# Kernel optimization log

Hardware: AMD Instinct MI355X
Metric: run time of the kernel (lower is better)

Reference implementation:

```python
import jax, jax.numpy as jnp
import numpy as np

B, C, H, W = 8, 256, 128, 128
KC, VC, HEADS = 256, 256, 2
HK, HV = KC // HEADS, VC // HEADS
EPS = 1e-5


def setup_inputs() -> dict:
    key = jax.random.key(0)
    ks = jax.random.split(key, 10)
    s = 0.02  # init scale for weights
    return {
        "x": jax.random.normal(ks[0], (B, C, H, W), jnp.float32),
        "bn_gamma": jnp.ones((C,), jnp.float32),
        "bn_beta": jnp.zeros((C,), jnp.float32),
        "wk": jax.random.normal(ks[1], (KC, C), jnp.float32) * s,
        "bk": jnp.zeros((KC,), jnp.float32),
        "wq": jax.random.normal(ks[2], (KC, C), jnp.float32) * s,
        "bq": jnp.zeros((KC,), jnp.float32),
        "wv": jax.random.normal(ks[3], (VC, C), jnp.float32) * s,
        "bv": jnp.zeros((VC,), jnp.float32),
        "w_fc1": jax.random.normal(ks[4], (HEADS, HEADS), jnp.float32) * 0.5,
        "b_fc1": jnp.zeros((HEADS,), jnp.float32),
        "w_fc2": jax.random.normal(ks[5], (HEADS, HEADS), jnp.float32) * 0.5,
        "b_fc2": jnp.zeros((HEADS,), jnp.float32),
        "w_se": jax.random.normal(ks[6], (HEADS,), jnp.float32) * 0.5,  # Conv2d(heads,1,1) weight
        "b_se": jnp.zeros((), jnp.float32),
        "w_rep": jax.random.normal(ks[7], (C, C), jnp.float32) * s,
        "b_rep": jnp.zeros((C,), jnp.float32),
    }


def reference(x, bn_gamma, bn_beta, wk, bk, wq, bq, wv, bv,
              w_fc1, b_fc1, w_fc2, b_fc2, w_se, b_se, w_rep, b_rep):
    n, c, h, w = x.shape
    s = h * w
    # BatchNorm2d (training-mode math: batch statistics over N,H,W)
    mean = x.mean(axis=(0, 2, 3))
    var = x.var(axis=(0, 2, 3))
    xn = (x - mean[None, :, None, None]) * jax.lax.rsqrt(var + EPS)[None, :, None, None]
    xn = xn * bn_gamma[None, :, None, None] + bn_beta[None, :, None, None]
    xr = xn.reshape(n, c, s)  # [B, C, HW]
    # 1x1 convs == per-pixel channel matmuls
    k = jnp.einsum('oc,bcs->bos', wk, xr) + bk[None, :, None]
    q = jnp.einsum('oc,bcs->bos', wq, xr) + bq[None, :, None]
    v = jnp.einsum('oc,bcs->bos', wv, xr) + bv[None, :, None]
    # split heads: [B, HEADS, hk, S]
    k = jax.nn.softmax(k.reshape(n, HEADS, HK, s), axis=-1)   # softmax over spatial
    q = jax.nn.softmax(q.reshape(n, HEADS, HK, s), axis=2)    # softmax over channel
    v = v.reshape(n, HEADS, HV, s)
    # linear-attention context: key @ value^T -> [B, HEADS, hk, hv]
    context = jnp.einsum('bnks,bnvs->bnkv', k, v)
    # SE block over head channel (in_channels = HEADS, reduction = 1)
    pooled = context.mean(axis=(2, 3))                              # [B, HEADS]
    gate = jax.nn.sigmoid(jax.nn.relu(pooled @ w_fc1.T + b_fc1) @ w_fc2.T + b_fc2)
    gated = context * gate[:, :, None, None]
    ctx = jnp.einsum('n,bnkv->bkv', w_se, gated) + b_se             # Conv2d(HEADS,1,1): [B, hk, hv]
    # second pass: ctx^T @ query per head, concat over heads -> [B, C, S]
    out = jnp.einsum('bkv,bnks->bnvs', ctx, q).reshape(n, c, s)
    out = jnp.einsum('oc,bcs->bos', w_rep, out) + b_rep[None, :, None]
    return out.reshape(n, c, h, w)
```

## Files before the change

### kernel.cpp

```cpp
#include <hip/hip_runtime.h>
#include <hip/hip_bf16.h>

#define BATCH 8
#define CH 256
#define SPAT 16384
#define TP 64
#define PITCH 272

typedef __attribute__((ext_vector_type(4))) float f32x4;
typedef __attribute__((ext_vector_type(8))) __bf16 bf16x8;
typedef __attribute__((ext_vector_type(4))) __bf16 bf16x4;

#define WS_ROWSUM  512
#define WS_POOLED  2560
#define WS_BKF     2576
#define WS_BQF     2832
#define WS_BVF     3088
#define WS_SUM     3344
#define WS_SSUM    3600
#define WS_CTX     4096
#define WS_MBF     266240
#define WS_WKBF    528384
#define WS_WQBF    561152
#define WS_WVBF    593920

__device__ __forceinline__ int lswz(int h) { return h ^ (((h >> 7) & 7) << 3); }

__device__ __forceinline__ void blockReduce2(float& a, float& b, volatile float* sm) {
    int lane = threadIdx.x & 63, w = threadIdx.x >> 6;
#pragma unroll
    for (int o = 32; o; o >>= 1) { a += __shfl_down(a, o); b += __shfl_down(b, o); }
    if (lane == 0) { sm[w] = a; sm[4 + w] = b; }
    __syncthreads();
    if (threadIdx.x == 0) {
        a = sm[0] + sm[1] + sm[2] + sm[3];
        b = sm[4] + sm[5] + sm[6] + sm[7];
    }
}

__global__ __launch_bounds__(256) void ea_bnstats(const float* __restrict__ x,
                                                  float* sums, float* ssums) {
    __shared__ float sm[8];
    int bi = blockIdx.x, c = bi >> 3, b = bi & 7;
    const float4* p = (const float4*)(x + (size_t)(b * CH + c) * SPAT);
    float sum = 0.f, ss = 0.f;
    for (int i = threadIdx.x; i < SPAT / 4; i += 256) {
        float4 v = p[i];
        sum += v.x + v.y + v.z + v.w;
        ss  += v.x * v.x + v.y * v.y + v.z * v.z + v.w * v.w;
    }
    blockReduce2(sum, ss, sm);
    if (threadIdx.x == 0) { atomicAdd(sums + c, sum); atomicAdd(ssums + c, ss); }
}

__global__ __launch_bounds__(256) void ea_fold(const float* __restrict__ wk, const float* __restrict__ wq,
        const float* __restrict__ wv, const float* __restrict__ bk, const float* __restrict__ bq,
        const float* __restrict__ bv, const float* __restrict__ gamma, const float* __restrict__ beta,
        const float* __restrict__ sums, const float* __restrict__ ssums,
        __bf16* wkb, __bf16* wqb, __bf16* wvb, float* bkf, float* bqf, float* bvf) {
    __shared__ float sm[12];
    int o = blockIdx.x, c = threadIdx.x;
    const float inv = 1.f / (float)(BATCH * SPAT);
    float mean = sums[c] * inv;
    float var  = ssums[c] * inv - mean * mean;
    float sc   = gamma[c] * rsqrtf(var + 1e-5f);
    float sh   = beta[c] - mean * sc;
    float k = wk[o * 256 + c], q = wq[o * 256 + c], v = wv[o * 256 + c];
    wkb[o * 256 + c] = (__bf16)(k * sc);
    wqb[o * 256 + c] = (__bf16)(q * sc);
    wvb[o * 256 + c] = (__bf16)(v * sc);
    float ak = k * sh, aq = q * sh, av = v * sh;
    int lane = c & 63, w = c >> 6;
#pragma unroll
    for (int off = 32; off; off >>= 1) {
        ak += __shfl_down(ak, off);
        aq += __shfl_down(aq, off);
        av += __shfl_down(av, off);
    }
    if (lane == 0) { sm[w] = ak; sm[4 + w] = aq; sm[8 + w] = av; }
    __syncthreads();
    if (c == 0) {
        bkf[o] = bk[o] + sm[0] + sm[1] + sm[2] + sm[3];
        bqf[o] = bq[o] + sm[4] + sm[5] + sm[6] + sm[7];
        bvf[o] = bv[o] + sm[8] + sm[9] + sm[10] + sm[11];
    }
}

__global__ __launch_bounds__(512, 2) void ea_kvctx(const float* __restrict__ x,
        const __bf16* __restrict__ wkb, const __bf16* __restrict__ wvb,
        const float* __restrict__ bkf, const float* __restrict__ bvf,
        float* __restrict__ ctx, float* __restrict__ rowsum) {
    __shared__ __bf16 Xl[2 * 64 * 256];
    __shared__ __bf16 Pl[256 * 64];
    __shared__ __bf16 Vl[256 * 64];
    const int bi = blockIdx.x, b = bi >> 5, chunk = bi & 31;
    const int t = threadIdx.x;
    const int lane = t & 63, wave = t >> 6, quad = lane >> 4, l15 = lane & 15;
    const int rbase = wave * 32;
    const int sl = t & 15, cg = t >> 4;
    const int xswz = (sl & 7) << 3;
    const float* xp0 = x + (size_t)(b * CH + cg * 8) * SPAT + chunk * 512 + 4 * sl;

    float bkr[2][4], bvr[2][4];
#pragma unroll
    for (int mt = 0; mt < 2; mt++)
#pragma unroll
        for (int r = 0; r < 4; r++) {
            int row = rbase + mt * 16 + quad * 4 + r;
            bkr[mt][r] = bkf[row];
            bvr[mt][r] = bvf[row];
        }

    const f32x4 z = {0.f, 0.f, 0.f, 0.f};
    f32x4 cacc[4][4];
#pragma unroll
    for (int mt = 0; mt < 4; mt++)
#pragma unroll
        for (int nt = 0; nt < 4; nt++) cacc[mt][nt] = z;
    float rs_acc[2][4] = {{0.f, 0.f, 0.f, 0.f}, {0.f, 0.f, 0.f, 0.f}};

    const int head = wave >> 2, rh = (wave >> 1) & 1, chh = wave & 1;
    const int prow0 = head * 128 + rh * 64, vrow0 = head * 128 + chh * 64;

    f32x4 xr[8];
#pragma unroll
    for (int i = 0; i < 8; i++) xr[i] = *(const f32x4*)(xp0 + (size_t)i * SPAT);
#pragma unroll
    for (int i = 0; i < 8; i++) {
        int ca = (cg * 8 + i) ^ xswz;
#pragma unroll
        for (int j = 0; j < 4; j++)
            Xl[(4 * sl + j) * 256 + ca] = (__bf16)xr[i][j];
    }
    __syncthreads();

    int buf = 0;
    for (int tt = 0; tt < 8; tt++) {
        if (tt < 7) {
            const float* xp = xp0 + (tt + 1) * 64;
#pragma unroll
            for (int i = 0; i < 8; i++) xr[i] = *(const f32x4*)(xp + (size_t)i * SPAT);
        }
        const __bf16* Xb = Xl + buf * (64 * 256);
        f32x4 ak[2][4], av[2][4];
#pragma unroll
        for (int mt = 0; mt < 2; mt++)
#pragma unroll
            for (int nt = 0; nt < 4; nt++) { ak[mt][nt] = z; av[mt][nt] = z; }
#pragma unroll 1
        for (int ks = 0; ks < 8; ks++) {
            int k0 = ks * 32 + quad * 8;
            bf16x8 bb[4];
#pragma unroll
            for (int nt = 0; nt < 4; nt++)
                bb[nt] = *(const bf16x8*)(Xb + (4 * l15 + nt) * 256 + (k0 ^ ((l15 & 7) << 3)));
            bf16x8 aK[2], aV[2];
#pragma unroll
            for (int mt = 0; mt < 2; mt++) {
                size_t off = (size_t)(rbase + mt * 16 + l15) * 256 + k0;
                aK[mt] = *(const bf16x8*)(wkb + off);
                aV[mt] = *(const bf16x8*)(wvb + off);
            }
#pragma unroll
            for (int mt = 0; mt < 2; mt++)
#pragma unroll
                for (int nt = 0; nt < 4; nt++) {
                    ak[mt][nt] = __builtin_amdgcn_mfma_f32_16x16x32_bf16(aK[mt], bb[nt], ak[mt][nt], 0, 0, 0);
                    av[mt][nt] = __builtin_amdgcn_mfma_f32_16x16x32_bf16(aV[mt], bb[nt], av[mt][nt], 0, 0, 0);
                }
        }
#pragma unroll
        for (int mt = 0; mt < 2; mt++)
#pragma unroll
            for (int r = 0; r < 4; r++) {
                int row = rbase + mt * 16 + quad * 4 + r;
                float bK = bkr[mt][r], bV = bvr[mt][r];
                float e0 = __expf(ak[mt][0][r] + bK);
                float e1 = __expf(ak[mt][1][r] + bK);
                float e2 = __expf(ak[mt][2][r] + bK);
                float e3 = __expf(ak[mt][3][r] + bK);
                rs_acc[mt][r] += e0 + e1 + e2 + e3;
                int pa = row * 64 + ((4 * l15) ^ ((row & 7) << 3));
                bf16x4 pk = {(__bf16)e0, (__bf16)e1, (__bf16)e2, (__bf16)e3};
                *(bf16x4*)(Pl + pa) = pk;
                bf16x4 vk = {(__bf16)(av[mt][0][r] + bV), (__bf16)(av[mt][1][r] + bV),
                             (__bf16)(av[mt][2][r] + bV), (__bf16)(av[mt][3][r] + bV)};
                *(bf16x4*)(Vl + pa) = vk;
            }
        __syncthreads();
        if (tt < 7) {
            __bf16* Xn = Xl + (buf ^ 1) * (64 * 256);
#pragma unroll
            for (int i = 0; i < 8; i++) {
                int ca = (cg * 8 + i) ^ xswz;
#pragma unroll
                for (int j = 0; j < 4; j++)
                    Xn[(4 * sl + j) * 256 + ca] = (__bf16)xr[i][j];
            }
        }
#pragma unroll
        for (int ks = 0; ks < 2; ks++) {
            int k0 = ks * 32 + quad * 8;
            bf16x8 pfr[4], vfr[4];
#pragma unroll
            for (int mt = 0; mt < 4; mt++) {
                int row = prow0 + mt * 16 + l15;
                pfr[mt] = *(const bf16x8*)(Pl + row * 64 + (k0 ^ ((row & 7) << 3)));
            }
#pragma unroll
            for (int nt = 0; nt < 4; nt++) {
                int row = vrow0 + nt * 16 + l15;
                vfr[nt] = *(const bf16x8*)(Vl + row * 64 + (k0 ^ ((row & 7) << 3)));
            }
#pragma unroll
            for (int mt = 0; mt < 4; mt++)
#pragma unroll
                for (int nt = 0; nt < 4; nt++)
                    cacc[mt][nt] = __builtin_amdgcn_mfma_f32_16x16x32_bf16(pfr[mt], vfr[nt], cacc[mt][nt], 0, 0, 0);
        }
        __syncthreads();
        buf ^= 1;
    }
#pragma unroll
    for (int mt = 0; mt < 2; mt++)
#pragma unroll
        for (int r = 0; r < 4; r++) {
            float v = rs_acc[mt][r];
            v += __shfl_xor(v, 1);
            v += __shfl_xor(v, 2);
            v += __shfl_xor(v, 4);
            v += __shfl_xor(v, 8);
            if (l15 == 0)
                atomicAdd(rowsum + b * CH + rbase + mt * 16 + quad * 4 + r, v);
        }
    float* cb = ctx + ((size_t)b * 2 + head) * 16384;
#pragma unroll
    for (int mt = 0; mt < 4; mt++)
#pragma unroll
        for (int nt = 0; nt < 4; nt++)
#pragma unroll
            for (int r = 0; r < 4; r++) {
                int kk = rh * 64 + mt * 16 + quad * 4 + r;
                int vv = chh * 64 + nt * 16 + l15;
                atomicAdd(cb + kk * 128 + vv, cacc[mt][nt][r]);
            }
}

__global__ void ea_normpool(float* ctx, const float* rowsum, float* pooled) {
    __shared__ float sm[8];
    int bi = blockIdx.x, b = bi >> 1, h = bi & 1;
    float* base = ctx + (size_t)bi * 16384;
    const float* rs = rowsum + b * CH + h * 128;
    float sum = 0.f, dummy = 0.f;
    for (int i = threadIdx.x; i < 16384; i += 256) {
        float v = base[i] / rs[i >> 7];
        base[i] = v;
        sum += v;
    }
    blockReduce2(sum, dummy, sm);
    if (threadIdx.x == 0) pooled[bi] = sum * (1.f / 16384.f);
}

__global__ __launch_bounds__(256) void ea_M(const float* ctx, const float* pooled,
                                            const float* wfc1, const float* bfc1,
                                            const float* wfc2, const float* bfc2,
                                            const float* wse, const float* bse,
                                            const float* wrep, __bf16* Mbf) {
    __shared__ float L[128 * 128];
    int bi = blockIdx.x, b = bi >> 3, h = (bi >> 2) & 1, strip = bi & 3;
    float p0 = pooled[b * 2], p1 = pooled[b * 2 + 1];
    float z10 = fmaxf(0.f, wfc1[0] * p0 + wfc1[1] * p1 + bfc1[0]);
    float z11 = fmaxf(0.f, wfc1[2] * p0 + wfc1[3] * p1 + bfc1[1]);
    float z20 = wfc2[0] * z10 + wfc2[1] * z11 + bfc2[0];
    float z21 = wfc2[2] * z10 + wfc2[3] * z11 + bfc2[1];
    float g0 = 1.f / (1.f + __expf(-z20)), g1 = 1.f / (1.f + __expf(-z21));
    float a0 = wse[0] * g0, a1 = wse[1] * g1, bs = bse[0];
    const float* c0 = ctx + (size_t)b * 2 * 16384;
    const float* c1 = c0 + 16384;
    for (int i = threadIdx.x; i < 16384; i += 256) L[i] = a0 * c0[i] + a1 * c1[i] + bs;
    __syncthreads();
    int o = strip * 64 + (threadIdx.x & 63), kb = (threadIdx.x >> 6) * 32;
    const float4* wr = (const float4*)(wrep + (size_t)o * 256 + h * 128);
    for (int kk = kb; kk < kb + 32; kk++) {
        const float4* Lr = (const float4*)(L + kk * 128);
        float acc = 0.f;
#pragma unroll 8
        for (int j = 0; j < 32; j++) {
            float4 w4 = wr[j];
            float4 l4 = Lr[j];
            acc += w4.x * l4.x + w4.y * l4.y + w4.z * l4.z + w4.w * l4.w;
        }
        Mbf[(size_t)(b * 256 + o) * 256 + h * 128 + kk] = (__bf16)acc;
    }
}

__device__ __forceinline__ void stage_x(const float* xb, __bf16* Xl, int t) {
    int l15 = t & 15, c0 = t >> 4;
    const float* xp = xb + l15 * 4;
    int hbase = (l15 * 4) * PITCH;
#pragma unroll
    for (int i = 0; i < 16; i++) {
        int c = c0 * 16 + i;
        float4 v = *(const float4*)(xp + (size_t)c * SPAT);
        Xl[lswz(hbase + c)]             = (__bf16)v.x;
        Xl[lswz(hbase + PITCH + c)]     = (__bf16)v.y;
        Xl[lswz(hbase + 2 * PITCH + c)] = (__bf16)v.z;
        Xl[lswz(hbase + 3 * PITCH + c)] = (__bf16)v.w;
    }
}

__device__ __forceinline__ void mm256(const __bf16* __restrict__ A, const __bf16* Xl,
                                      int WB, int quad, int l15, f32x4 (&acc)[4][4]) {
#pragma unroll 2
    for (int ks = 0; ks < 8; ks++) {
        int k0 = ks * 32;
        bf16x8 a[4];
#pragma unroll
        for (int mt = 0; mt < 4; mt++)
            a[mt] = *(const bf16x8*)(A + (WB + mt * 16 + l15) * 256 + k0 + quad * 8);
        bf16x8 bb[4];
#pragma unroll
        for (int nt = 0; nt < 4; nt++)
            bb[nt] = *(const bf16x8*)(Xl + lswz((4 * l15 + nt) * PITCH + k0 + quad * 8));
#pragma unroll
        for (int mt = 0; mt < 4; mt++)
#pragma unroll
            for (int nt = 0; nt < 4; nt++)
                acc[mt][nt] = __builtin_amdgcn_mfma_f32_16x16x32_bf16(a[mt], bb[nt], acc[mt][nt], 0, 0, 0);
    }
}

__global__ __launch_bounds__(256) void ea_final(const float* __restrict__ x,
        const __bf16* __restrict__ wqb, const float* __restrict__ bqf,
        const __bf16* __restrict__ Mbf, const float* __restrict__ brep, float* __restrict__ out) {
    __shared__ __bf16 X[TP * PITCH];
    __shared__ __bf16 Q[TP * PITCH];
    __shared__ float psum[256];
    __shared__ float rcp[TP * 2];
    int bi = blockIdx.x, b = bi >> 8, s0 = (bi & 255) * TP, t = threadIdx.x;
    stage_x(x + (size_t)b * CH * SPAT + s0, X, t);
    __syncthreads();

    int lane = t & 63, wave = t >> 6, quad = lane >> 4, l15 = lane & 15, WB = wave * 64;
    const f32x4 z = {0.f, 0.f, 0.f, 0.f};

    {
        f32x4 acc[4][4];
#pragma unroll
        for (int mt = 0; mt < 4; mt++)
#pragma unroll
            for (int nt = 0; nt < 4; nt++) acc[mt][nt] = z;
        mm256(wqb, X, WB, quad, l15, acc);
#pragma unroll
        for (int mt = 0; mt < 4; mt++) {
            int row0 = WB + mt * 16 + quad * 4;
#pragma unroll
            for (int nt = 0; nt < 4; nt++) {
                bf16x4 qk;
#pragma unroll
                for (int r = 0; r < 4; r++)
                    qk[r] = (__bf16)__expf(acc[mt][nt][r] + bqf[row0 + r]);
                *(bf16x4*)(Q + lswz((4 * l15 + nt) * PITCH + row0)) = qk;
            }
        }
    }
    __syncthreads();
    {
        int px = t & 63, hh = (t >> 6) & 1, part = t >> 7;
        int cb = hh * 128 + part * 64;
        float s = 0.f;
#pragma unroll
        for (int j = 0; j < 8; j++) {
            bf16x8 qv = *(const bf16x8*)(Q + lswz(px * PITCH + cb + j * 8));
#pragma unroll
            for (int e = 0; e < 8; e++) s += (float)qv[e];
        }
        psum[t] = s;
    }
    __syncthreads();
    if (t < 128) {
        float tot = psum[t] + psum[t + 128];
        rcp[(t & 63) * 2 + (t >> 6)] = 1.f / tot;
    }
    __syncthreads();
#pragma unroll 2
    for (int e = t; e < TP * 32; e += 256) {
        int px = e >> 5, cc = (e & 31) * 8;
        float sc = rcp[px * 2 + (cc >> 7)];
        int h = lswz(px * PITCH + cc);
        bf16x8 qv = *(const bf16x8*)(Q + h);
        bf16x8 qo;
#pragma unroll
        for (int j2 = 0; j2 < 8; j2++) qo[j2] = (__bf16)((float)qv[j2] * sc);
        *(bf16x8*)(Q + h) = qo;
    }
    __syncthreads();
    {
        f32x4 acc[4][4];
#pragma unroll
        for (int mt = 0; mt < 4; mt++)
#pragma unroll
            for (int nt = 0; nt < 4; nt++) acc[mt][nt] = z;
        mm256(Mbf + (size_t)b * 65536, Q, WB, quad, l15, acc);
#pragma unroll
        for (int mt = 0; mt < 4; mt++) {
            int row0 = WB + mt * 16 + quad * 4;
#pragma unroll
            for (int r = 0; r < 4; r++) {
                int row = row0 + r;
                float bs = brep[row];
                f32x4 o4 = {acc[mt][0][r] + bs, acc[mt][1][r] + bs,
                            acc[mt][2][r] + bs, acc[mt][3][r] + bs};
                *(f32x4*)(out + (size_t)(b * CH + row) * SPAT + s0 + 4 * l15) = o4;
            }
        }
    }
}

extern "C" void kernel_launch(void* const* d_in, const int* in_sizes, int n_in,
                              void* d_out, int out_size, void* d_ws, size_t ws_size,
                              hipStream_t stream) {
    (void)in_sizes; (void)n_in; (void)out_size; (void)ws_size;
    const float* x     = (const float*)d_in[0];
    const float* gamma = (const float*)d_in[1];
    const float* beta  = (const float*)d_in[2];
    const float* wk    = (const float*)d_in[3];
    const float* bk    = (const float*)d_in[4];
    const float* wq    = (const float*)d_in[5];
    const float* bq    = (const float*)d_in[6];
    const float* wv    = (const float*)d_in[7];
    const float* bv    = (const float*)d_in[8];
    const float* wfc1  = (const float*)d_in[9];
    const float* bfc1  = (const float*)d_in[10];
    const float* wfc2  = (const float*)d_in[11];
    const float* bfc2  = (const float*)d_in[12];
    const float* wse   = (const float*)d_in[13];
    const float* bse   = (const float*)d_in[14];
    const float* wrep  = (const float*)d_in[15];
    const float* brep  = (const float*)d_in[16];

    float* ws = (float*)d_ws;
    __bf16* wkb = (__bf16*)(ws + WS_WKBF);
    __bf16* wqb = (__bf16*)(ws + WS_WQBF);
    __bf16* wvb = (__bf16*)(ws + WS_WVBF);
    __bf16* Mbf = (__bf16*)(ws + WS_MBF);
    float* out = (float*)d_out;

    hipMemsetAsync((void*)(ws + WS_ROWSUM), 0,
                   (size_t)(WS_MBF - WS_ROWSUM) * sizeof(float), stream);
    ea_bnstats<<<2048, 256, 0, stream>>>(x, ws + WS_SUM, ws + WS_SSUM);
    ea_fold<<<256, 256, 0, stream>>>(wk, wq, wv, bk, bq, bv, gamma, beta,
                                     ws + WS_SUM, ws + WS_SSUM,
                                     wkb, wqb, wvb, ws + WS_BKF, ws + WS_BQF, ws + WS_BVF);
    ea_kvctx<<<256, 512, 0, stream>>>(x, wkb, wvb, ws + WS_BKF, ws + WS_BVF,
                                      ws + WS_CTX, ws + WS_ROWSUM);
    ea_normpool<<<16, 256, 0, stream>>>(ws + WS_CTX, ws + WS_ROWSUM, ws + WS_POOLED);
    ea_M<<<64, 256, 0, stream>>>(ws + WS_CTX, ws + WS_POOLED, wfc1, bfc1, wfc2, bfc2,
                                 wse, bse, wrep, Mbf);
    ea_final<<<2048, 256, 0, stream>>>(x, wqb, ws + WS_BQF, Mbf, brep, out);
}
```

Baseline: 604.9 us.

## Replace context atomics with per-chunk partials and a separate reduction kernel

The kv-context kernel now writes per-chunk context partials with vectorized stores into the output buffer, which serves as scratch. This replaces the many scalar float atomicAdds to a shared context. A new reduction kernel sums the 32 chunks, normalizes by the row sums, and accumulates the pooled mean atomically. It also swaps the MFMA operand order so accumulators map to contiguous stores, moves the next-tile global prefetch and LDS staging later in the loop, and unrolls the k-loop by 2. The cost is extra memory traffic for 16 MB of partials and one more kernel launch.

```diff
diff --git a/kernel.cpp b/kernel.cpp
--- a/kernel.cpp
+++ b/kernel.cpp
@@ -89,7 +89,7 @@
 __global__ __launch_bounds__(512, 2) void ea_kvctx(const float* __restrict__ x,
         const __bf16* __restrict__ wkb, const __bf16* __restrict__ wvb,
         const float* __restrict__ bkf, const float* __restrict__ bvf,
-        float* __restrict__ ctx, float* __restrict__ rowsum) {
+        float* __restrict__ ctxpart, float* __restrict__ rowsum) {
     __shared__ __bf16 Xl[2 * 64 * 256];
     __shared__ __bf16 Pl[256 * 64];
     __shared__ __bf16 Vl[256 * 64];
@@ -114,9 +114,9 @@
     const f32x4 z = {0.f, 0.f, 0.f, 0.f};
     f32x4 cacc[4][4];
 #pragma unroll
-    for (int mt = 0; mt < 4; mt++)
-#pragma unroll
-        for (int nt = 0; nt < 4; nt++) cacc[mt][nt] = z;
+    for (int vt = 0; vt < 4; vt++)
+#pragma unroll
+        for (int kt = 0; kt < 4; kt++) cacc[vt][kt] = z;
     float rs_acc[2][4] = {{0.f, 0.f, 0.f, 0.f}, {0.f, 0.f, 0.f, 0.f}};
 
     const int head = wave >> 2, rh = (wave >> 1) & 1, chh = wave & 1;
@@ -136,18 +136,13 @@
 
     int buf = 0;
     for (int tt = 0; tt < 8; tt++) {
-        if (tt < 7) {
-            const float* xp = xp0 + (tt + 1) * 64;
-#pragma unroll
-            for (int i = 0; i < 8; i++) xr[i] = *(const f32x4*)(xp + (size_t)i * SPAT);
-        }
         const __bf16* Xb = Xl + buf * (64 * 256);
         f32x4 ak[2][4], av[2][4];
 #pragma unroll
         for (int mt = 0; mt < 2; mt++)
 #pragma unroll
             for (int nt = 0; nt < 4; nt++) { ak[mt][nt] = z; av[mt][nt] = z; }
-#pragma unroll 1
+#pragma unroll 2
         for (int ks = 0; ks < 8; ks++) {
             int k0 = ks * 32 + quad * 8;
             bf16x8 bb[4];
@@ -168,6 +163,11 @@
                     ak[mt][nt] = __builtin_amdgcn_mfma_f32_16x16x32_bf16(aK[mt], bb[nt], ak[mt][nt], 0, 0, 0);
                     av[mt][nt] = __builtin_amdgcn_mfma_f32_16x16x32_bf16(aV[mt], bb[nt], av[mt][nt], 0, 0, 0);
                 }
+        }
+        if (tt < 7) {
+            const float* xp = xp0 + (tt + 1) * 64;
+#pragma unroll
+            for (int i = 0; i < 8; i++) xr[i] = *(const f32x4*)(xp + (size_t)i * SPAT);
         }
 #pragma unroll
         for (int mt = 0; mt < 2; mt++)
@@ -188,35 +188,35 @@
                 *(bf16x4*)(Vl + pa) = vk;
             }
         __syncthreads();
-        if (tt < 7) {
-            __bf16* Xn = Xl + (buf ^ 1) * (64 * 256);
-#pragma unroll
-            for (int i = 0; i < 8; i++) {
-                int ca = (cg * 8 + i) ^ xswz;
-#pragma unroll
-                for (int j = 0; j < 4; j++)
-                    Xn[(4 * sl + j) * 256 + ca] = (__bf16)xr[i][j];
-            }
-        }
 #pragma unroll
         for (int ks = 0; ks < 2; ks++) {
             int k0 = ks * 32 + quad * 8;
             bf16x8 pfr[4], vfr[4];
 #pragma unroll
-            for (int mt = 0; mt < 4; mt++) {
-                int row = prow0 + mt * 16 + l15;
-                pfr[mt] = *(const bf16x8*)(Pl + row * 64 + (k0 ^ ((row & 7) << 3)));
-            }
-#pragma unroll
-            for (int nt = 0; nt < 4; nt++) {
-                int row = vrow0 + nt * 16 + l15;
-                vfr[nt] = *(const bf16x8*)(Vl + row * 64 + (k0 ^ ((row & 7) << 3)));
-            }
-#pragma unroll
-            for (int mt = 0; mt < 4; mt++)
-#pragma unroll
-                for (int nt = 0; nt < 4; nt++)
-                    cacc[mt][nt] = __builtin_amdgcn_mfma_f32_16x16x32_bf16(pfr[mt], vfr[nt], cacc[mt][nt], 0, 0, 0);
+            for (int kt = 0; kt < 4; kt++) {
+                int row = prow0 + kt * 16 + l15;
+                pfr[kt] = *(const bf16x8*)(Pl + row * 64 + (k0 ^ ((row & 7) << 3)));
+            }
+#pragma unroll
+            for (int vt = 0; vt < 4; vt++) {
+                int row = vrow0 + vt * 16 + l15;
+                vfr[vt] = *(const bf16x8*)(Vl + row * 64 + (k0 ^ ((row & 7) << 3)));
+            }
+#pragma unroll
+            for (int vt = 0; vt < 4; vt++)
+#pragma unroll
+                for (int kt = 0; kt < 4; kt++)
+                    cacc[vt][kt] = __builtin_amdgcn_mfma_f32_16x16x32_bf16(vfr[vt], pfr[kt], cacc[vt][kt], 0, 0, 0);
+        }
+        if (tt < 7) {
+            __bf16* Xn = Xl + (buf ^ 1) * (64 * 256);
+#pragma unroll
+            for (int i = 0; i < 8; i++) {
+                int ca = (cg * 8 + i) ^ xswz;
+#pragma unroll
+                for (int j = 0; j < 4; j++)
+                    Xn[(4 * sl + j) * 256 + ca] = (__bf16)xr[i][j];
+            }
         }
         __syncthreads();
         buf ^= 1;
@@ -233,32 +233,36 @@
             if (l15 == 0)
                 atomicAdd(rowsum + b * CH + rbase + mt * 16 + quad * 4 + r, v);
         }
-    float* cb = ctx + ((size_t)b * 2 + head) * 16384;
-#pragma unroll
-    for (int mt = 0; mt < 4; mt++)
-#pragma unroll
-        for (int nt = 0; nt < 4; nt++)
-#pragma unroll
-            for (int r = 0; r < 4; r++) {
-                int kk = rh * 64 + mt * 16 + quad * 4 + r;
-                int vv = chh * 64 + nt * 16 + l15;
-                atomicAdd(cb + kk * 128 + vv, cacc[mt][nt][r]);
-            }
-}
-
-__global__ void ea_normpool(float* ctx, const float* rowsum, float* pooled) {
+    float* pbase = ctxpart + (((size_t)(b * 32 + chunk)) * 2 + head) * 16384;
+#pragma unroll
+    for (int vt = 0; vt < 4; vt++)
+#pragma unroll
+        for (int kt = 0; kt < 4; kt++) {
+            int kk = rh * 64 + kt * 16 + l15;
+            int vv = chh * 64 + vt * 16 + quad * 4;
+            *(f32x4*)(pbase + kk * 128 + vv) = cacc[vt][kt];
+        }
+}
+
+__global__ __launch_bounds__(256) void ea_ctxred(const float* __restrict__ part,
+        const float* __restrict__ rowsum, float* __restrict__ ctx, float* __restrict__ pooled) {
     __shared__ float sm[8];
-    int bi = blockIdx.x, b = bi >> 1, h = bi & 1;
-    float* base = ctx + (size_t)bi * 16384;
-    const float* rs = rowsum + b * CH + h * 128;
-    float sum = 0.f, dummy = 0.f;
-    for (int i = threadIdx.x; i < 16384; i += 256) {
-        float v = base[i] / rs[i >> 7];
-        base[i] = v;
-        sum += v;
-    }
-    blockReduce2(sum, dummy, sm);
-    if (threadIdx.x == 0) pooled[bi] = sum * (1.f / 16384.f);
+    int bi = blockIdx.x, b = bi >> 5, h = (bi >> 4) & 1, ks = bi & 15;
+    int t = threadIdx.x;
+    int kk = ks * 8 + (t >> 5), vv = (t & 31) * 4;
+    const float* p0 = part + (((size_t)b * 32) * 2 + h) * 16384 + (size_t)kk * 128 + vv;
+    f32x4 acc = {0.f, 0.f, 0.f, 0.f};
+#pragma unroll 4
+    for (int c = 0; c < 32; c++) {
+        f32x4 v = *(const f32x4*)(p0 + (size_t)c * 32768);
+        acc[0] += v[0]; acc[1] += v[1]; acc[2] += v[2]; acc[3] += v[3];
+    }
+    float inv = 1.f / rowsum[b * CH + h * 128 + kk];
+    f32x4 o = {acc[0] * inv, acc[1] * inv, acc[2] * inv, acc[3] * inv};
+    *(f32x4*)(ctx + ((size_t)b * 2 + h) * 16384 + (size_t)kk * 128 + vv) = o;
+    float s = o[0] + o[1] + o[2] + o[3], d = 0.f;
+    blockReduce2(s, d, sm);
+    if (t == 0) atomicAdd(pooled + b * 2 + h, s);
 }
 
 __global__ __launch_bounds__(256) void ea_M(const float* ctx, const float* pooled,
@@ -268,7 +272,7 @@
                                             const float* wrep, __bf16* Mbf) {
     __shared__ float L[128 * 128];
     int bi = blockIdx.x, b = bi >> 3, h = (bi >> 2) & 1, strip = bi & 3;
-    float p0 = pooled[b * 2], p1 = pooled[b * 2 + 1];
+    float p0 = pooled[b * 2] * (1.f / 16384.f), p1 = pooled[b * 2 + 1] * (1.f / 16384.f);
     float z10 = fmaxf(0.f, wfc1[0] * p0 + wfc1[1] * p1 + bfc1[0]);
     float z11 = fmaxf(0.f, wfc1[2] * p0 + wfc1[3] * p1 + bfc1[1]);
     float z20 = wfc2[0] * z10 + wfc2[1] * z11 + bfc2[0];
@@ -444,17 +448,19 @@
     __bf16* wqb = (__bf16*)(ws + WS_WQBF);
     __bf16* wvb = (__bf16*)(ws + WS_WVBF);
     __bf16* Mbf = (__bf16*)(ws + WS_MBF);
+
+    float* ctxpart = (float*)d_out;
     float* out = (float*)d_out;
 
     hipMemsetAsync((void*)(ws + WS_ROWSUM), 0,
-                   (size_t)(WS_MBF - WS_ROWSUM) * sizeof(float), stream);
+                   (size_t)(WS_CTX - WS_ROWSUM) * sizeof(float), stream);
     ea_bnstats<<<2048, 256, 0, stream>>>(x, ws + WS_SUM, ws + WS_SSUM);
     ea_fold<<<256, 256, 0, stream>>>(wk, wq, wv, bk, bq, bv, gamma, beta,
                                      ws + WS_SUM, ws + WS_SSUM,
                                      wkb, wqb, wvb, ws + WS_BKF, ws + WS_BQF, ws + WS_BVF);
     ea_kvctx<<<256, 512, 0, stream>>>(x, wkb, wvb, ws + WS_BKF, ws + WS_BVF,
-                                      ws + WS_CTX, ws + WS_ROWSUM);
-    ea_normpool<<<16, 256, 0, stream>>>(ws + WS_CTX, ws + WS_ROWSUM, ws + WS_POOLED);
+                                      ctxpart, ws + WS_ROWSUM);
+    ea_ctxred<<<256, 256, 0, stream>>>(ctxpart, ws + WS_ROWSUM, ws + WS_CTX, ws + WS_POOLED);
     ea_M<<<64, 256, 0, stream>>>(ws + WS_CTX, ws + WS_POOLED, wfc1, bfc1, wfc2, bfc2,
                                  wse, bse, wrep, Mbf);
     ea_final<<<2048, 256, 0, stream>>>(x, wqb, ws + WS_BQF, Mbf, brep, out);
```

After: 593.7 us. Within noise of the previous version (-1.9%).
